# Optimization experiments

Hardware: AMD Instinct MI355X
Metric: run time of the kernel (lower is better)

## Reference

```python
import jax, jax.numpy as jnp
import numpy as np
import math

B, S, E, R = 128, 16, 512, 500  # batch, seq_len, emb_size, relation_num


def setup_inputs() -> dict:
    key = jax.random.key(0)
    ks = jax.random.split(key, 12)
    s = 1.0 / math.sqrt(E)
    emb = jax.random.normal(ks[0], (R + 1, E), jnp.float32) * s
    emb = emb.at[R].set(0.0)  # padding_idx row is zero in torch
    w_ih = jax.random.normal(ks[1], (4 * E, E), jnp.float32) * s
    w_hh = jax.random.normal(ks[2], (4 * E, E), jnp.float32) * s
    b_ih = jax.random.normal(ks[3], (4 * E,), jnp.float32) * s
    b_hh = jax.random.normal(ks[4], (4 * E,), jnp.float32) * s
    fc_w = jax.random.normal(ks[5], (1, E), jnp.float32) * s
    fc_b = jax.random.normal(ks[6], (1,), jnp.float32) * s
    fcq_w = jax.random.normal(ks[7], (E, E), jnp.float32) * s
    fcq_b = jax.random.normal(ks[8], (E,), jnp.float32) * s
    fck_w = jax.random.normal(ks[9], (E, E), jnp.float32) * s
    fck_b = jax.random.normal(ks[10], (E,), jnp.float32) * s
    tokens = jax.random.randint(ks[11], (B, S), 0, R)  # avoid padding idx R
    return dict(tokens=tokens, emb=emb, w_ih=w_ih, w_hh=w_hh, b_ih=b_ih,
                b_hh=b_hh, fc_w=fc_w, fc_b=fc_b, fcq_w=fcq_w, fcq_b=fcq_b,
                fck_w=fck_w, fck_b=fck_b)


def _lstm_pair(x, w_ih, w_hh, b):
    # x: [..., 2, E]; 2-step LSTM from zero state, return final hidden [..., E]
    def cell(xt, h, c):
        g = xt @ w_ih.T + h @ w_hh.T + b
        i, f, gg, o = jnp.split(g, 4, axis=-1)  # torch gate order i,f,g,o
        c = jax.nn.sigmoid(f) * c + jax.nn.sigmoid(i) * jnp.tanh(gg)
        return jax.nn.sigmoid(o) * jnp.tanh(c), c
    z = jnp.zeros_like(x[..., 0, :])
    h1, c1 = cell(x[..., 0, :], z, z)
    h2, _ = cell(x[..., 1, :], h1, c1)
    return h2


def _attention(x, rel_emb, fcq_w, fcq_b, fck_w, fck_b):
    # x: [B,q,E]; keys = [relation embeddings ; x] -> scores [B,q,R+q]
    b = x.shape[0]
    rel = jnp.broadcast_to(rel_emb[None], (b,) + rel_emb.shape)
    kin = jnp.concatenate([rel, x], axis=1)
    k = kin @ fck_w.T + fck_b
    q = x @ fcq_w.T + fcq_b
    return jnp.einsum('bqe,bke->bqk', q, k) / math.sqrt(E)


def _entropy(scores):
    lp = jax.nn.log_softmax(scores, axis=-1)
    return -jnp.sum(jnp.exp(lp) * lp, axis=-1)


def reference(tokens, emb, w_ih, w_hh, b_ih, b_hh, fc_w, fc_b,
              fcq_w, fcq_b, fck_w, fck_b):
    b_lstm = b_ih + b_hh
    rel_emb = emb[:R]  # relation embeddings used as attention keys/values
    cur = emb[tokens]  # [B,S,E]
    bidx = jnp.arange(B)
    losses = []
    for L in range(S, 1, -1):  # lengths processed: S, S-1, ..., 2
        if L > 2:
            # all adjacent pairs, batched 2-step LSTM: [B, L-1, E]
            pairs = jnp.stack([cur[:, :-1], cur[:, 1:]], axis=2)
            h = _lstm_pair(pairs, w_ih, w_hh, b_lstm)
            sc = jax.nn.sigmoid(h @ fc_w.T + fc_b)[..., 0]  # [B, L-1]
            sel = jnp.argmax(sc, axis=-1)  # [B]
            selected = jnp.take_along_axis(h, sel[:, None, None], axis=1)  # [B,1,E]
            scores = _attention(selected, rel_emb, fcq_w, fcq_b, fck_w, fck_b)
            losses.append(_entropy(scores))  # [B,1]
            # weightedAverage: mask is all-False for seq_len==1, plain softmax
            prob = jax.nn.softmax(scores, axis=-1)  # [B,1,R+1]
            all_emb = jnp.concatenate(
                [jnp.broadcast_to(rel_emb[None], (B, R, E)), selected], axis=1)
            merged = jnp.einsum('bqk,bke->bqe', prob, all_emb)[:, 0]  # [B,E]
            # output = inputs.detach().clone(); write merged at sel; drop row sel+1
            base = jax.lax.stop_gradient(cur)
            base = base.at[bidx, sel].set(merged)
            j = jnp.arange(L - 1)[None, :]
            src = j + (j > sel[:, None]).astype(j.dtype)
            cur = jnp.take_along_axis(base, src[:, :, None], axis=1)  # [B,L-1,E]
        else:  # L == 2: plain LSTM over the two tokens
            h = _lstm_pair(cur, w_ih, w_hh, b_lstm)  # [B,E]
            cur = h[:, None, :]
            losses.append(jnp.zeros((B, 1), cur.dtype))
    scores_f = _attention(cur, rel_emb, fcq_w, fcq_b, fck_w, fck_b)  # [B,1,R+1]
    losses.append(_entropy(scores_f))
    loss_tensor = jnp.concatenate(losses, axis=-1)  # [B,S]
    return scores_f[:, 0], loss_tensor
```

## Files before the change

### kernel.cpp

```cpp
#include <hip/hip_runtime.h>
#include <hip/hip_bf16.h>

#define BB 128
#define SS 16
#define EE 512
#define RR 500
#define G4 2048
#define OUT0 64128
#define NSC 501
#define NPAIR 2047
#define NSU 1012

__device__ __forceinline__ float sigm(float x) { return 1.f / (1.f + expf(-x)); }

__device__ float g_blstm[G4];
__device__ float g_blstmr[G4];
__device__ float g_wihr[G4 * EE];
__device__ float g_whhr[G4 * EE];
__device__ float g_fcw[EE + 4];
__device__ float g_qbias[1024];
__device__ float g_Krel[RR * EE];
__device__ float g_cur[BB * SS * EE];
__device__ float g_G[BB * SS * G4];
__device__ float g_h1[BB * SS * EE];
__device__ float g_c1[BB * SS * EE];
__device__ float g_h2[BB * SS * EE];
__device__ float g_sc[BB * SS];
__device__ float g_ent[BB * SS];
__device__ int   g_sel[BB];
__device__ int   g_ord[BB * SS];
__device__ float g_fckwT[EE * EE];
__device__ float g_W2[RR * EE];
__device__ float g_Mx[EE * EE];
__device__ float g_c2[RR + 4];
__device__ float g_v1[EE];
__device__ float g_c0[1];
__device__ float g_su[BB * NSU];

__global__ void k_prep(const float* __restrict__ bih, const float* __restrict__ bhh,
                       const float* __restrict__ fcwv, const float* __restrict__ fcbv,
                       const float* __restrict__ fcqb, const float* __restrict__ fckb) {
    int i = blockIdx.x * blockDim.x + threadIdx.x;
    if (i < G4) g_blstm[i] = bih[i] + bhh[i];
    if (i < EE) {
        g_fcw[i] = fcwv[i];
        g_qbias[i] = fcqb[i];
        g_qbias[EE + i] = fckb[i];
    }
    if (i == 0) g_fcw[EE] = fcbv[0];
    if (i < BB * SS) g_ord[i] = i;
}

__global__ void k_reord(const float* __restrict__ wih, const float* __restrict__ whh) {
    int i = blockIdx.x * blockDim.x + threadIdx.x;
    if (i >= G4 * EE) return;
    int n = i >> 9;
    int k = i & (EE - 1);
    int e = n & (EE - 1);
    int gate = n >> 9;
    int np = 4 * e + gate;
    g_wihr[(size_t)np * EE + k] = wih[i];
    g_whhr[(size_t)np * EE + k] = whh[i];
    if (k == 0) g_blstmr[np] = g_blstm[n];
}

__global__ void k_gather(const int* __restrict__ tok, const float* __restrict__ emb) {
    int i = blockIdx.x * blockDim.x + threadIdx.x;
    if (i >= BB * SS * EE) return;
    int e = i & (EE - 1);
    int r = i >> 9;
    int t = tok[r];
    g_cur[i] = emb[(size_t)t * EE + e];
}

__global__ void k_tr(const float* __restrict__ fckw) {
    int i = blockIdx.x * blockDim.x + threadIdx.x;
    if (i >= EE * EE) return;
    int ep = i >> 9;
    int f = i & (EE - 1);
    g_fckwT[(size_t)f * EE + ep] = fckw[(size_t)ep * EE + f];
}

__global__ __launch_bounds__(512) void k_vprep(const float* __restrict__ fcqw, const float* __restrict__ fckw) {
    __shared__ float sh[512];
    int t = threadIdx.x;
    int blk = blockIdx.x;
    if (blk == 0) {
        float acc = 0.f;
        for (int ep = 0; ep < EE; ep++)
            acc += g_qbias[ep] * fckw[(size_t)ep * EE + t] + g_qbias[EE + ep] * fcqw[(size_t)ep * EE + t];
        g_v1[t] = acc;
    } else if (blk == 1) {
        sh[t] = g_qbias[t] * g_qbias[EE + t];
        __syncthreads();
        for (int s = 256; s > 0; s >>= 1) { if (t < s) sh[t] += sh[t + s]; __syncthreads(); }
        if (t == 0) g_c0[0] = sh[0];
    } else {
        int k = blk - 2;
        sh[t] = g_Krel[(size_t)k * EE + t] * g_qbias[t];
        __syncthreads();
        for (int s = 256; s > 0; s >>= 1) { if (t < s) sh[t] += sh[t + s]; __syncthreads(); }
        if (t == 0) g_c2[k] = sh[0];
    }
}

#define TM 32
#define TN 64
#define TK 32
__device__ __forceinline__ void gemm_dev(
    const float* __restrict__ A, int lda,
    const float* __restrict__ W, int ldw, int wtrans,
    const float* __restrict__ bias, const float* __restrict__ Dadd, int ldd,
    float* __restrict__ C, int ldc, int M, int N, int K)
{
    __shared__ __align__(16) float As[TK][TM + 2];
    __shared__ __align__(16) float Ws[TK][TN + 4];
    int tid = threadIdx.x;
    int mt = blockIdx.y * TM;
    int nt = blockIdx.x * TN;
    int tr = tid >> 4;
    int tc = tid & 15;
    float acc[2][4] = {{0.f,0.f,0.f,0.f},{0.f,0.f,0.f,0.f}};

    int ea = tid * 4;
    int ra = ea >> 5;
    int ka = ea & 31;
    int gmA = mt + ra;
    bool rokA = gmA < M;
    int ew = tid * 8;
    int rw = ew >> 5;
    int kw = ew & 31;
    int gnW = nt + rw;
    bool rokW = gnW < N;

    for (int kt = 0; kt < K; kt += TK) {
        #pragma unroll
        for (int i = 0; i < 4; i++) {
            int gk = kt + ka + i;
            float v = 0.f;
            if (rokA && gk < K) v = A[(size_t)gmA * lda + gk];
            As[ka + i][ra] = v;
        }
        #pragma unroll
        for (int i = 0; i < 8; i++) {
            int gk = kt + kw + i;
            float v = 0.f;
            if (rokW && gk < K)
                v = wtrans ? W[(size_t)gk * ldw + gnW] : W[(size_t)gnW * ldw + gk];
            Ws[kw + i][rw] = v;
        }
        __syncthreads();
        #pragma unroll
        for (int kk = 0; kk < TK; kk++) {
            const float2 a = *(const float2*)&As[kk][2 * tr];
            const float4 w = *(const float4*)&Ws[kk][4 * tc];
            acc[0][0] += a.x * w.x; acc[0][1] += a.x * w.y; acc[0][2] += a.x * w.z; acc[0][3] += a.x * w.w;
            acc[1][0] += a.y * w.x; acc[1][1] += a.y * w.y; acc[1][2] += a.y * w.z; acc[1][3] += a.y * w.w;
        }
        __syncthreads();
    }
    #pragma unroll
    for (int i = 0; i < 2; i++) {
        int gm = mt + 2 * tr + i;
        if (gm >= M) continue;
        #pragma unroll
        for (int j = 0; j < 4; j++) {
            int gn = nt + 4 * tc + j;
            if (gn >= N) continue;
            float v = (i == 0) ? ((j == 0) ? acc[0][0] : (j == 1) ? acc[0][1] : (j == 2) ? acc[0][2] : acc[0][3])
                               : ((j == 0) ? acc[1][0] : (j == 1) ? acc[1][1] : (j == 2) ? acc[1][2] : acc[1][3]);
            if (bias) v += bias[gn];
            if (Dadd) v += Dadd[(size_t)gm * ldd + gn];
            C[(size_t)gm * ldc + gn] = v;
        }
    }
}

#define UM 128
#define UN 128
#define UK 32
template<int MODE>
__global__ __launch_bounds__(256) void kg_bigF() {
    __shared__ __align__(16) float As[UK][UM + 4];
    __shared__ __align__(16) float Ws[UK][UN + 4];
    const float* __restrict__ A = (MODE == 0) ? g_cur : g_h1;
    const float* __restrict__ W = (MODE == 0) ? g_wihr : g_whhr;
    const int M = (MODE == 0) ? (BB * SS) : NPAIR;
    int tid = threadIdx.x;
    int mt = blockIdx.y * UM;
    int nt = blockIdx.x * UN;
    int tr = tid >> 4;
    int tc = tid & 15;
    float acc[8][8] = {};

    int ra = tid & 127;
    int ka = (tid >> 7) << 4;
    int gmA = mt + ra;
    bool rokA = gmA < M;
    const float* Arow = A + (size_t)(rokA ? gmA : 0) * EE;
    const float* Wrow = W + (size_t)(nt + ra) * EE;

    float4 pa[4] = {{0,0,0,0},{0,0,0,0},{0,0,0,0},{0,0,0,0}};
    float4 pw[4];
    #pragma unroll
    for (int j = 0; j < 4; j++) {
        if (rokA) pa[j] = *(const float4*)&Arow[ka + 4 * j];
        pw[j] = *(const float4*)&Wrow[ka + 4 * j];
    }

    for (int kt = 0; kt < EE; kt += UK) {
        __syncthreads();
        #pragma unroll
        for (int j = 0; j < 4; j++) {
            As[ka + 4 * j + 0][ra] = pa[j].x;
            As[ka + 4 * j + 1][ra] = pa[j].y;
            As[ka + 4 * j + 2][ra] = pa[j].z;
            As[ka + 4 * j + 3][ra] = pa[j].w;
            Ws[ka + 4 * j + 0][ra] = pw[j].x;
            Ws[ka + 4 * j + 1][ra] = pw[j].y;
            Ws[ka + 4 * j + 2][ra] = pw[j].z;
            Ws[ka + 4 * j + 3][ra] = pw[j].w;
        }
        __syncthreads();
        if (kt + UK < EE) {
            int k2 = kt + UK + ka;
            #pragma unroll
            for (int j = 0; j < 4; j++) {
                if (rokA) pa[j] = *(const float4*)&Arow[k2 + 4 * j];
                pw[j] = *(const float4*)&Wrow[k2 + 4 * j];
            }
        }
        #pragma unroll
        for (int kk = 0; kk < UK; kk++) {
            const float4 aA = *(const float4*)&As[kk][4 * tr];
            const float4 aB = *(const float4*)&As[kk][64 + 4 * tr];
            const float4 wA = *(const float4*)&Ws[kk][4 * tc];
            const float4 wB = *(const float4*)&Ws[kk][64 + 4 * tc];
            const float am[8] = {aA.x, aA.y, aA.z, aA.w, aB.x, aB.y, aB.z, aB.w};
            const float wn[8] = {wA.x, wA.y, wA.z, wA.w, wB.x, wB.y, wB.z, wB.w};
            #pragma unroll
            for (int i = 0; i < 8; i++)
                #pragma unroll
                for (int j = 0; j < 8; j++)
                    acc[i][j] += am[i] * wn[j];
        }
    }

    int c0 = nt + 4 * tc;
    int c1c = c0 + 64;
    int e0 = (nt >> 2) + tc;
    #pragma unroll
    for (int ri = 0; ri < 8; ri++) {
        int row = (ri < 4) ? (4 * tr + ri) : (60 + 4 * tr + ri);
        int gm = mt + row;
        if (gm >= M) continue;
        float q0x = acc[ri][0], q0y = acc[ri][1], q0z = acc[ri][2], q0w = acc[ri][3];
        float q1x = acc[ri][4], q1y = acc[ri][5], q1z = acc[ri][6], q1w = acc[ri][7];
        if (MODE == 0) {
            const float4 b0 = *(const float4*)&g_blstmr[c0];
            const float4 b1 = *(const float4*)&g_blstmr[c1c];
            q0x += b0.x; q0y += b0.y; q0z += b0.z; q0w += b0.w;
            q1x += b1.x; q1y += b1.y; q1z += b1.z; q1w += b1.w;
            float4 o0 = {q0x, q0y, q0z, q0w};
            float4 o1 = {q1x, q1y, q1z, q1w};
            *(float4*)&g_G[(size_t)gm * G4 + c0]  = o0;
            *(float4*)&g_G[(size_t)gm * G4 + c1c] = o1;
            float cA = sigm(q0x) * tanhf(q0z);
            g_c1[(size_t)gm * EE + e0] = cA;
            g_h1[(size_t)gm * EE + e0] = sigm(q0w) * tanhf(cA);
            float cB = sigm(q1x) * tanhf(q1z);
            g_c1[(size_t)gm * EE + e0 + 16] = cB;
            g_h1[(size_t)gm * EE + e0 + 16] = sigm(q1w) * tanhf(cB);
        } else {
            const float4 d0 = *(const float4*)&g_G[(size_t)(gm + 1) * G4 + c0];
            const float4 d1 = *(const float4*)&g_G[(size_t)(gm + 1) * G4 + c1c];
            q0x += d0.x; q0y += d0.y; q0z += d0.z; q0w += d0.w;
            q1x += d1.x; q1y += d1.y; q1z += d1.z; q1w += d1.w;
            float c1a = g_c1[(size_t)gm * EE + e0];
            float c1b = g_c1[(size_t)gm * EE + e0 + 16];
            float cA = sigm(q0y) * c1a + sigm(q0x) * tanhf(q0z);
            g_h2[(size_t)gm * EE + e0] = sigm(q0w) * tanhf(cA);
            float cB = sigm(q1y) * c1b + sigm(q1x) * tanhf(q1z);
            g_h2[(size_t)gm * EE + e0 + 16] = sigm(q1w) * tanhf(cB);
        }
    }
}

__global__ __launch_bounds__(256) void kg_Krel(const float* __restrict__ emb, const float* __restrict__ fckw) {
    gemm_dev(emb, EE, fckw, EE, 0, g_qbias + EE, nullptr, 0, g_Krel, EE, RR, EE, EE);
}
__global__ __launch_bounds__(256) void kg_W2(const float* __restrict__ fcqw) {
    gemm_dev(g_Krel, EE, fcqw, EE, 1, nullptr, nullptr, 0, g_W2, EE, RR, EE, EE);
}
__global__ __launch_bounds__(256) void kg_Mx(const float* __restrict__ fcqw) {
    gemm_dev(g_fckwT, EE, fcqw, EE, 1, nullptr, nullptr, 0, g_Mx, EE, EE, EE, EE);
}

__global__ __launch_bounds__(256) void k_scI() {
    int m = blockIdx.x;
    int t = threadIdx.x;
    __shared__ float red[256];
    const float* h = g_h2 + (size_t)m * EE;
    float part = h[t] * g_fcw[t] + h[t + 256] * g_fcw[t + 256];
    red[t] = part;
    __syncthreads();
    for (int s = 128; s > 0; s >>= 1) { if (t < s) red[t] += red[t + s]; __syncthreads(); }
    if (t == 0) g_sc[m] = red[0];
}

__global__ __launch_bounds__(256) void k_scP(int L) {
    int m = blockIdx.x;
    int b = m >> 1;
    int tcand = m & 1;
    int s = g_sel[b];
    int p = s - 1 + tcand;
    bool valid = tcand == 0 ? (s >= 1) : (s <= L - 3);
    if (!valid) return;
    int physL = g_ord[b * SS + p];
    int t = threadIdx.x;
    __shared__ float red[256];
    const float* h = g_h2 + (size_t)physL * EE;
    float part = h[t] * g_fcw[t] + h[t + 256] * g_fcw[t + 256];
    red[t] = part;
    __syncthreads();
    for (int s2 = 128; s2 > 0; s2 >>= 1) { if (t < s2) red[t] += red[t + s2]; __syncthreads(); }
    if (t == 0) g_sc[b * SS + p] = red[0];
}

__global__ __launch_bounds__(256) void kg_su(int P) {
    __shared__ __align__(16) float As[TK][TM + 2];
    __shared__ __align__(16) float Ws[TK][TN + 4];
    __shared__ int s_phys[TM];
    int tid = threadIdx.x;
    int mt = blockIdx.y * TM;
    int nt = blockIdx.x * TN;
    int tr = tid >> 4;
    int tc = tid & 15;
    float acc[2][4] = {{0.f,0.f,0.f,0.f},{0.f,0.f,0.f,0.f}};

    if (tid < TM) {
        int b = mt + tid;
        float best = -1e30f; int bi = 0;
        for (int p = 0; p < P; p++) {
            float v = g_sc[b * SS + p];
            if (v > best) { best = v; bi = p; }
        }
        s_phys[tid] = g_ord[b * SS + bi];
        if (blockIdx.x == 0) g_sel[b] = bi;
    }
    __syncthreads();

    int ea = tid * 4;
    int ra = ea >> 5;
    int ka = ea & 31;
    int physA = s_phys[ra];
    int ew = tid * 8;
    int rw = ew >> 5;
    int kw = ew & 31;
    int gnW = nt + rw;
    bool rokW = gnW < NSU;
    const float* Wrow = nullptr;
    if (rokW) Wrow = (gnW < RR) ? (g_W2 + (size_t)gnW * EE) : (g_Mx + (size_t)(gnW - RR) * EE);

    for (int kt = 0; kt < EE; kt += TK) {
        #pragma unroll
        for (int i = 0; i < 4; i++)
            As[ka + i][ra] = g_h2[(size_t)physA * EE + kt + ka + i];
        #pragma unroll
        for (int i = 0; i < 8; i++)
            Ws[kw + i][rw] = rokW ? Wrow[kt + kw + i] : 0.f;
        __syncthreads();
        #pragma unroll
        for (int kk = 0; kk < TK; kk++) {
            const float2 a = *(const float2*)&As[kk][2 * tr];
            const float4 w = *(const float4*)&Ws[kk][4 * tc];
            acc[0][0] += a.x * w.x; acc[0][1] += a.x * w.y; acc[0][2] += a.x * w.z; acc[0][3] += a.x * w.w;
            acc[1][0] += a.y * w.x; acc[1][1] += a.y * w.y; acc[1][2] += a.y * w.z; acc[1][3] += a.y * w.w;
        }
        __syncthreads();
    }
    #pragma unroll
    for (int i = 0; i < 2; i++) {
        int gm = mt + 2 * tr + i;
        #pragma unroll
        for (int j = 0; j < 4; j++) {
            int gn = nt + 4 * tc + j;
            if (gn >= NSU) continue;
            float v = (i == 0) ? ((j == 0) ? acc[0][0] : (j == 1) ? acc[0][1] : (j == 2) ? acc[0][2] : acc[0][3])
                               : ((j == 0) ? acc[1][0] : (j == 1) ? acc[1][1] : (j == 2) ? acc[1][2] : acc[1][3]);
            g_su[(size_t)gm * NSU + gn] = v + (gn < RR ? g_c2[gn] : 0.f);
        }
    }
}

__global__ __launch_bounds__(256) void kg_GiF() {
    __shared__ __align__(16) float As[TK][TM + 2];
    __shared__ __align__(16) float Ws[TK][TN + 4];
    __shared__ int s_phys[TM];
    int tid = threadIdx.x;
    int mt = blockIdx.y * TM;
    int nt = blockIdx.x * TN;
    int tr = tid >> 4;
    int tc = tid & 15;
    float acc[2][4] = {{0.f,0.f,0.f,0.f},{0.f,0.f,0.f,0.f}};

    if (tid < TM) {
        int b = mt + tid;
        s_phys[tid] = g_ord[b * SS + g_sel[b]];
    }
    __syncthreads();

    int ea = tid * 4;
    int ra = ea >> 5;
    int ka = ea & 31;
    int physA = s_phys[ra];
    int ew = tid * 8;
    int rw = ew >> 5;
    int kw = ew & 31;
    int gnW = nt + rw;

    for (int kt = 0; kt < EE; kt += TK) {
        #pragma unroll
        for (int i = 0; i < 4; i++)
            As[ka + i][ra] = g_cur[(size_t)physA * EE + kt + ka + i];
        #pragma unroll
        for (int i = 0; i < 8; i++)
            Ws[kw + i][rw] = g_wihr[(size_t)gnW * EE + kt + kw + i];
        __syncthreads();
        #pragma unroll
        for (int kk = 0; kk < TK; kk++) {
            const float2 a = *(const float2*)&As[kk][2 * tr];
            const float4 w = *(const float4*)&Ws[kk][4 * tc];
            acc[0][0] += a.x * w.x; acc[0][1] += a.x * w.y; acc[0][2] += a.x * w.z; acc[0][3] += a.x * w.w;
            acc[1][0] += a.y * w.x; acc[1][1] += a.y * w.y; acc[1][2] += a.y * w.z; acc[1][3] += a.y * w.w;
        }
        __syncthreads();
    }
    int c0 = nt + 4 * tc;
    int e0 = (nt >> 2) + tc;
    const float4 b4 = *(const float4*)&g_blstmr[c0];
    #pragma unroll
    for (int i = 0; i < 2; i++) {
        int phys = s_phys[2 * tr + i];
        float qx = acc[i][0] + b4.x;
        float qy = acc[i][1] + b4.y;
        float qz = acc[i][2] + b4.z;
        float qw = acc[i][3] + b4.w;
        float4 o = {qx, qy, qz, qw};
        *(float4*)&g_G[(size_t)phys * G4 + c0] = o;
        float cA = sigm(qx) * tanhf(qz);
        g_c1[(size_t)phys * EE + e0] = cA;
        g_h1[(size_t)phys * EE + e0] = sigm(qw) * tanhf(cA);
    }
}

__global__ __launch_bounds__(256) void kg_g2iF(int L) {
    __shared__ __align__(16) float As[TK][TM + 2];
    __shared__ __align__(16) float Ws[TK][TN + 4];
    __shared__ int s_physA[TM];
    __shared__ int s_physD[TM];
    __shared__ int s_val[TM];
    int tid = threadIdx.x;
    int mt = blockIdx.y * TM;
    int nt = blockIdx.x * TN;
    int tr = tid >> 4;
    int tc = tid & 15;
    float acc[2][4] = {{0.f,0.f,0.f,0.f},{0.f,0.f,0.f,0.f}};

    if (tid < TM) {
        int gm = mt + tid;
        int b = gm >> 1;
        int tcand = gm & 1;
        int s = g_sel[b];
        int p = min(max(s - 1 + tcand, 0), 14);
        s_physA[tid] = g_ord[b * SS + p];
        s_physD[tid] = g_ord[b * SS + p + 1];
        s_val[tid] = tcand == 0 ? (s >= 1) : (s <= L - 3);
    }
    __syncthreads();

    int ea = tid * 4;
    int ra = ea >> 5;
    int ka = ea & 31;
    int physA = s_physA[ra];
    int ew = tid * 8;
    int rw = ew >> 5;
    int kw = ew & 31;
    int gnW = nt + rw;

    for (int kt = 0; kt < EE; kt += TK) {
        #pragma unroll
        for (int i = 0; i < 4; i++)
            As[ka + i][ra] = g_h1[(size_t)physA * EE + kt + ka + i];
        #pragma unroll
        for (int i = 0; i < 8; i++)
            Ws[kw + i][rw] = g_whhr[(size_t)gnW * EE + kt + kw + i];
        __syncthreads();
        #pragma unroll
        for (int kk = 0; kk < TK; kk++) {
            const float2 a = *(const float2*)&As[kk][2 * tr];
            const float4 w = *(const float4*)&Ws[kk][4 * tc];
            acc[0][0] += a.x * w.x; acc[0][1] += a.x * w.y; acc[0][2] += a.x * w.z; acc[0][3] += a.x * w.w;
            acc[1][0] += a.y * w.x; acc[1][1] += a.y * w.y; acc[1][2] += a.y * w.z; acc[1][3] += a.y * w.w;
        }
        __syncthreads();
    }
    int c0 = nt + 4 * tc;
    int e0 = (nt >> 2) + tc;
    #pragma unroll
    for (int i = 0; i < 2; i++) {
        int r = 2 * tr + i;
        if (!s_val[r]) continue;
        int pA = s_physA[r];
        int pD = s_physD[r];
        const float4 d4 = *(const float4*)&g_G[(size_t)pD * G4 + c0];
        float qx = acc[i][0] + d4.x;
        float qy = acc[i][1] + d4.y;
        float qz = acc[i][2] + d4.z;
        float qw = acc[i][3] + d4.w;
        float c1v = g_c1[(size_t)pA * EE + e0];
        float cA = sigm(qy) * c1v + sigm(qx) * tanhf(qz);
        g_h2[(size_t)pA * EE + e0] = sigm(qw) * tanhf(cA);
    }
}

__global__ __launch_bounds__(512) void k_smu(int col, int finalFlag, int L,
                                             const float* __restrict__ emb, float* __restrict__ out) {
    int b = blockIdx.x;
    int t = threadIdx.x;
    __shared__ float sh[512];
    __shared__ float srow[NSC];
    __shared__ float s_p500;
    const float* su = g_su + (size_t)b * NSU;
    int s = g_sel[b];
    int phys = g_ord[b * SS + s];
    const float* h2row = g_h2 + (size_t)phys * EE;
    const float isq = 0.044194173824159216f;

    float hv = h2row[t];
    sh[t] = hv * (su[RR + t] + g_v1[t]);
    __syncthreads();
    for (int ss = 256; ss > 0; ss >>= 1) { if (t < ss) sh[t] += sh[t + ss]; __syncthreads(); }
    if (t == 0) srow[RR] = (sh[0] + g_c0[0]) * isq;
    __syncthreads();
    if (t < RR) srow[t] = su[t] * isq;
    __syncthreads();
    float mx = (t < NSC) ? srow[t] : -1e30f;
    sh[t] = mx; __syncthreads();
    for (int ss = 256; ss > 0; ss >>= 1) { if (t < ss) sh[t] = fmaxf(sh[t], sh[t + ss]); __syncthreads(); }
    mx = sh[0]; __syncthreads();
    float zp = (t < NSC) ? expf(srow[t] - mx) : 0.f;
    sh[t] = zp; __syncthreads();
    for (int ss = 256; ss > 0; ss >>= 1) { if (t < ss) sh[t] += sh[t + ss]; __syncthreads(); }
    float lse = mx + logf(sh[0]);
    __syncthreads();
    float p = (t < NSC) ? expf(srow[t] - lse) : 0.f;
    float ep = (t < NSC) ? p * (lse - srow[t]) : 0.f;
    if (finalFlag && t < NSC) out[(size_t)b * NSC + t] = srow[t];
    sh[t] = ep; __syncthreads();
    for (int ss = 256; ss > 0; ss >>= 1) { if (t < ss) sh[t] += sh[t + ss]; __syncthreads(); }
    if (finalFlag) {
        if (t < 16) {
            float v = (t == 15) ? sh[0] : ((t == 14) ? 0.f : g_ent[b * SS + t]);
            out[OUT0 + b * 16 + t] = v;
        }
        return;
    }
    if (t == 0) g_ent[b * SS + col] = sh[0];

    __syncthreads();
    if (t < NSC) srow[t] = p;
    if (t == RR) s_p500 = p;
    __syncthreads();
    float macc = 0.f;
    #pragma unroll 4
    for (int k = 0; k < RR; k++) macc += srow[k] * emb[(size_t)k * EE + t];
    g_cur[(size_t)phys * EE + t] = macc + s_p500 * hv;
    if (t == 0) {
        for (int j = s + 1; j <= L - 2; j++) g_ord[b * SS + j] = g_ord[b * SS + j + 1];
        for (int pp = s + 1; pp <= L - 3; pp++) g_sc[b * SS + pp] = g_sc[b * SS + pp + 1];
    }
}

extern "C" void kernel_launch(void* const* d_in, const int* in_sizes, int n_in,
                              void* d_out, int out_size, void* d_ws, size_t ws_size,
                              hipStream_t stream) {
    const int*   tokens = (const int*)d_in[0];
    const float* emb    = (const float*)d_in[1];
    const float* wih    = (const float*)d_in[2];
    const float* whh    = (const float*)d_in[3];
    const float* bih    = (const float*)d_in[4];
    const float* bhh    = (const float*)d_in[5];
    const float* fcwv   = (const float*)d_in[6];
    const float* fcbv   = (const float*)d_in[7];
    const float* fcqw   = (const float*)d_in[8];
    const float* fcqb   = (const float*)d_in[9];
    const float* fckw   = (const float*)d_in[10];
    const float* fckb   = (const float*)d_in[11];
    float* out = (float*)d_out;

    auto grid32 = [](int M, int N) { return dim3((unsigned)((N + TN - 1) / TN), (unsigned)((M + TM - 1) / TM)); };

    k_prep<<<dim3(8), dim3(256), 0, stream>>>(bih, bhh, fcwv, fcbv, fcqb, fckb);
    k_reord<<<dim3((G4 * EE) / 256), dim3(256), 0, stream>>>(wih, whh);
    kg_Krel<<<grid32(RR, EE), dim3(256), 0, stream>>>(emb, fckw);
    k_tr<<<dim3((EE * EE + 255) / 256), dim3(256), 0, stream>>>(fckw);
    kg_W2<<<grid32(RR, EE), dim3(256), 0, stream>>>(fcqw);
    kg_Mx<<<grid32(EE, EE), dim3(256), 0, stream>>>(fcqw);
    k_vprep<<<dim3(502), dim3(512), 0, stream>>>(fcqw, fckw);
    k_gather<<<dim3((BB * SS * EE + 255) / 256), dim3(256), 0, stream>>>(tokens, emb);

    kg_bigF<0><<<dim3(16, 16), dim3(256), 0, stream>>>();
    kg_bigF<1><<<dim3(16, 16), dim3(256), 0, stream>>>();
    k_scI<<<dim3(NPAIR), dim3(256), 0, stream>>>();

    for (int L = SS; L >= 3; L--) {
        kg_su<<<grid32(BB, NSU), dim3(256), 0, stream>>>(L - 1);
        k_smu<<<dim3(BB), dim3(512), 0, stream>>>(SS - L, 0, L, emb, out);
        kg_GiF<<<grid32(BB, G4), dim3(256), 0, stream>>>();
        kg_g2iF<<<grid32(2 * BB, G4), dim3(256), 0, stream>>>(L);
        k_scP<<<dim3(2 * BB), dim3(256), 0, stream>>>(L);
    }

    kg_su<<<grid32(BB, NSU), dim3(256), 0, stream>>>(1);
    k_smu<<<dim3(BB), dim3(512), 0, stream>>>(15, 1, 2, emb, out);

    (void)in_sizes; (void)n_in; (void)out_size; (void)d_ws; (void)ws_size;
}
```

Before: 1.953 ms.

## Vectorize and register-prefetch GEMM tile loads, halve bigF N-tile

Replaces the scalar, strided global loads in the shared 32x64 GEMM helper and the per-step gate/score GEMMs with float4 loads. These are prefetched into registers for the next K-tile while the current tile is being computed. The fcq weight is pre-transposed once so every GEMM reads W row-major, which removes the strided transposed-load path. The big LSTM input GEMM moves from a 128x128 to a 128x64 tile, doubling block count to improve occupancy at the cost of more A-tile reloads.

```diff
diff --git a/kernel.cpp b/kernel.cpp
--- a/kernel.cpp
+++ b/kernel.cpp
@@ -30,6 +30,7 @@
 __device__ int   g_sel[BB];
 __device__ int   g_ord[BB * SS];
 __device__ float g_fckwT[EE * EE];
+__device__ float g_fcqwT[EE * EE];
 __device__ float g_W2[RR * EE];
 __device__ float g_Mx[EE * EE];
 __device__ float g_c2[RR + 4];
@@ -73,12 +74,13 @@
     g_cur[i] = emb[(size_t)t * EE + e];
 }
 
-__global__ void k_tr(const float* __restrict__ fckw) {
+__global__ void k_tr(const float* __restrict__ fckw, const float* __restrict__ fcqw) {
     int i = blockIdx.x * blockDim.x + threadIdx.x;
     if (i >= EE * EE) return;
     int ep = i >> 9;
     int f = i & (EE - 1);
     g_fckwT[(size_t)f * EE + ep] = fckw[(size_t)ep * EE + f];
+    g_fcqwT[(size_t)f * EE + ep] = fcqw[(size_t)ep * EE + f];
 }
 
 __global__ __launch_bounds__(512) void k_vprep(const float* __restrict__ fcqw, const float* __restrict__ fckw) {
@@ -109,7 +111,7 @@
 #define TK 32
 __device__ __forceinline__ void gemm_dev(
     const float* __restrict__ A, int lda,
-    const float* __restrict__ W, int ldw, int wtrans,
+    const float* __restrict__ W, int ldw,
     const float* __restrict__ bias, const float* __restrict__ Dadd, int ldd,
     float* __restrict__ C, int ldc, int M, int N, int K)
 {
@@ -127,29 +129,27 @@
     int ka = ea & 31;
     int gmA = mt + ra;
     bool rokA = gmA < M;
+    const float* Arow = A + (size_t)(rokA ? gmA : 0) * lda;
     int ew = tid * 8;
     int rw = ew >> 5;
     int kw = ew & 31;
     int gnW = nt + rw;
     bool rokW = gnW < N;
+    const float* Wrow = W + (size_t)(rokW ? gnW : 0) * ldw;
+
+    float4 pa = {0,0,0,0}, pw0 = {0,0,0,0}, pw1 = {0,0,0,0};
+    if (rokA) pa = *(const float4*)&Arow[ka];
+    if (rokW) { pw0 = *(const float4*)&Wrow[kw]; pw1 = *(const float4*)&Wrow[kw + 4]; }
 
     for (int kt = 0; kt < K; kt += TK) {
-        #pragma unroll
-        for (int i = 0; i < 4; i++) {
-            int gk = kt + ka + i;
-            float v = 0.f;
-            if (rokA && gk < K) v = A[(size_t)gmA * lda + gk];
-            As[ka + i][ra] = v;
-        }
-        #pragma unroll
-        for (int i = 0; i < 8; i++) {
-            int gk = kt + kw + i;
-            float v = 0.f;
-            if (rokW && gk < K)
-                v = wtrans ? W[(size_t)gk * ldw + gnW] : W[(size_t)gnW * ldw + gk];
-            Ws[kw + i][rw] = v;
-        }
-        __syncthreads();
+        As[ka + 0][ra] = pa.x; As[ka + 1][ra] = pa.y; As[ka + 2][ra] = pa.z; As[ka + 3][ra] = pa.w;
+        Ws[kw + 0][rw] = pw0.x; Ws[kw + 1][rw] = pw0.y; Ws[kw + 2][rw] = pw0.z; Ws[kw + 3][rw] = pw0.w;
+        Ws[kw + 4][rw] = pw1.x; Ws[kw + 5][rw] = pw1.y; Ws[kw + 6][rw] = pw1.z; Ws[kw + 7][rw] = pw1.w;
+        __syncthreads();
+        if (kt + TK < K) {
+            if (rokA) pa = *(const float4*)&Arow[kt + TK + ka];
+            if (rokW) { pw0 = *(const float4*)&Wrow[kt + TK + kw]; pw1 = *(const float4*)&Wrow[kt + TK + kw + 4]; }
+        }
         #pragma unroll
         for (int kk = 0; kk < TK; kk++) {
             const float2 a = *(const float2*)&As[kk][2 * tr];
@@ -177,7 +177,7 @@
 }
 
 #define UM 128
-#define UN 128
+#define UN 64
 #define UK 32
 template<int MODE>
 __global__ __launch_bounds__(256) void kg_bigF() {
@@ -191,109 +191,97 @@
     int nt = blockIdx.x * UN;
     int tr = tid >> 4;
     int tc = tid & 15;
-    float acc[8][8] = {};
+    float acc[8][4] = {};
 
     int ra = tid & 127;
     int ka = (tid >> 7) << 4;
     int gmA = mt + ra;
     bool rokA = gmA < M;
     const float* Arow = A + (size_t)(rokA ? gmA : 0) * EE;
-    const float* Wrow = W + (size_t)(nt + ra) * EE;
-
-    float4 pa[4] = {{0,0,0,0},{0,0,0,0},{0,0,0,0},{0,0,0,0}};
-    float4 pw[4];
+    int rw = tid & 63;
+    int kw = (tid >> 6) << 3;
+    const float* Wrow = W + (size_t)(nt + rw) * EE;
+
+    float4 pa[4] = {};
+    float4 pw[2];
     #pragma unroll
-    for (int j = 0; j < 4; j++) {
-        if (rokA) pa[j] = *(const float4*)&Arow[ka + 4 * j];
-        pw[j] = *(const float4*)&Wrow[ka + 4 * j];
-    }
+    for (int j = 0; j < 4; j++) if (rokA) pa[j] = *(const float4*)&Arow[ka + 4 * j];
+    #pragma unroll
+    for (int j = 0; j < 2; j++) pw[j] = *(const float4*)&Wrow[kw + 4 * j];
 
     for (int kt = 0; kt < EE; kt += UK) {
-        __syncthreads();
         #pragma unroll
         for (int j = 0; j < 4; j++) {
             As[ka + 4 * j + 0][ra] = pa[j].x;
             As[ka + 4 * j + 1][ra] = pa[j].y;
             As[ka + 4 * j + 2][ra] = pa[j].z;
             As[ka + 4 * j + 3][ra] = pa[j].w;
-            Ws[ka + 4 * j + 0][ra] = pw[j].x;
-            Ws[ka + 4 * j + 1][ra] = pw[j].y;
-            Ws[ka + 4 * j + 2][ra] = pw[j].z;
-            Ws[ka + 4 * j + 3][ra] = pw[j].w;
+        }
+        #pragma unroll
+        for (int j = 0; j < 2; j++) {
+            Ws[kw + 4 * j + 0][rw] = pw[j].x;
+            Ws[kw + 4 * j + 1][rw] = pw[j].y;
+            Ws[kw + 4 * j + 2][rw] = pw[j].z;
+            Ws[kw + 4 * j + 3][rw] = pw[j].w;
         }
         __syncthreads();
         if (kt + UK < EE) {
-            int k2 = kt + UK + ka;
+            int k2 = kt + UK;
             #pragma unroll
-            for (int j = 0; j < 4; j++) {
-                if (rokA) pa[j] = *(const float4*)&Arow[k2 + 4 * j];
-                pw[j] = *(const float4*)&Wrow[k2 + 4 * j];
-            }
+            for (int j = 0; j < 4; j++) if (rokA) pa[j] = *(const float4*)&Arow[k2 + ka + 4 * j];
+            #pragma unroll
+            for (int j = 0; j < 2; j++) pw[j] = *(const float4*)&Wrow[k2 + kw + 4 * j];
         }
         #pragma unroll
         for (int kk = 0; kk < UK; kk++) {
             const float4 aA = *(const float4*)&As[kk][4 * tr];
             const float4 aB = *(const float4*)&As[kk][64 + 4 * tr];
-            const float4 wA = *(const float4*)&Ws[kk][4 * tc];
-            const float4 wB = *(const float4*)&Ws[kk][64 + 4 * tc];
+            const float4 w4 = *(const float4*)&Ws[kk][4 * tc];
             const float am[8] = {aA.x, aA.y, aA.z, aA.w, aB.x, aB.y, aB.z, aB.w};
-            const float wn[8] = {wA.x, wA.y, wA.z, wA.w, wB.x, wB.y, wB.z, wB.w};
+            const float wn[4] = {w4.x, w4.y, w4.z, w4.w};
             #pragma unroll
             for (int i = 0; i < 8; i++)
                 #pragma unroll
-                for (int j = 0; j < 8; j++)
+                for (int j = 0; j < 4; j++)
                     acc[i][j] += am[i] * wn[j];
         }
+        __syncthreads();
     }
 
     int c0 = nt + 4 * tc;
-    int c1c = c0 + 64;
     int e0 = (nt >> 2) + tc;
     #pragma unroll
     for (int ri = 0; ri < 8; ri++) {
         int row = (ri < 4) ? (4 * tr + ri) : (60 + 4 * tr + ri);
         int gm = mt + row;
         if (gm >= M) continue;
-        float q0x = acc[ri][0], q0y = acc[ri][1], q0z = acc[ri][2], q0w = acc[ri][3];
-        float q1x = acc[ri][4], q1y = acc[ri][5], q1z = acc[ri][6], q1w = acc[ri][7];
+        float qx = acc[ri][0], qy = acc[ri][1], qz = acc[ri][2], qw = acc[ri][3];
         if (MODE == 0) {
-            const float4 b0 = *(const float4*)&g_blstmr[c0];
-            const float4 b1 = *(const float4*)&g_blstmr[c1c];
-            q0x += b0.x; q0y += b0.y; q0z += b0.z; q0w += b0.w;
-            q1x += b1.x; q1y += b1.y; q1z += b1.z; q1w += b1.w;
-            float4 o0 = {q0x, q0y, q0z, q0w};
-            float4 o1 = {q1x, q1y, q1z, q1w};
-            *(float4*)&g_G[(size_t)gm * G4 + c0]  = o0;
-            *(float4*)&g_G[(size_t)gm * G4 + c1c] = o1;
-            float cA = sigm(q0x) * tanhf(q0z);
+            const float4 b4 = *(const float4*)&g_blstmr[c0];
+            qx += b4.x; qy += b4.y; qz += b4.z; qw += b4.w;
+            float4 o = {qx, qy, qz, qw};
+            *(float4*)&g_G[(size_t)gm * G4 + c0] = o;
+            float cA = sigm(qx) * tanhf(qz);
             g_c1[(size_t)gm * EE + e0] = cA;
-            g_h1[(size_t)gm * EE + e0] = sigm(q0w) * tanhf(cA);
-            float cB = sigm(q1x) * tanhf(q1z);
-            g_c1[(size_t)gm * EE + e0 + 16] = cB;
-            g_h1[(size_t)gm * EE + e0 + 16] = sigm(q1w) * tanhf(cB);
+            g_h1[(size_t)gm * EE + e0] = sigm(qw) * tanhf(cA);
         } else {
-            const float4 d0 = *(const float4*)&g_G[(size_t)(gm + 1) * G4 + c0];
-            const float4 d1 = *(const float4*)&g_G[(size_t)(gm + 1) * G4 + c1c];
-            q0x += d0.x; q0y += d0.y; q0z += d0.z; q0w += d0.w;
-            q1x += d1.x; q1y += d1.y; q1z += d1.z; q1w += d1.w;
-            float c1a = g_c1[(size_t)gm * EE + e0];
-            float c1b = g_c1[(size_t)gm * EE + e0 + 16];
-            float cA = sigm(q0y) * c1a + sigm(q0x) * tanhf(q0z);
-            g_h2[(size_t)gm * EE + e0] = sigm(q0w) * tanhf(cA);
-            float cB = sigm(q1y) * c1b + sigm(q1x) * tanhf(q1z);
-            g_h2[(size_t)gm * EE + e0 + 16] = sigm(q1w) * tanhf(cB);
+            const float4 d4 = *(const float4*)&g_G[(size_t)(gm + 1) * G4 + c0];
+            qx += d4.x; qy += d4.y; qz += d4.z; qw += d4.w;
+            float c1v = g_c1[(size_t)gm * EE + e0];
+            float cA = sigm(qy) * c1v + sigm(qx) * tanhf(qz);
+            g_h2[(size_t)gm * EE + e0] = sigm(qw) * tanhf(cA);
         }
     }
 }
 
 __global__ __launch_bounds__(256) void kg_Krel(const float* __restrict__ emb, const float* __restrict__ fckw) {
-    gemm_dev(emb, EE, fckw, EE, 0, g_qbias + EE, nullptr, 0, g_Krel, EE, RR, EE, EE);
-}
-__global__ __launch_bounds__(256) void kg_W2(const float* __restrict__ fcqw) {
-    gemm_dev(g_Krel, EE, fcqw, EE, 1, nullptr, nullptr, 0, g_W2, EE, RR, EE, EE);
-}
-__global__ __launch_bounds__(256) void kg_Mx(const float* __restrict__ fcqw) {
-    gemm_dev(g_fckwT, EE, fcqw, EE, 1, nullptr, nullptr, 0, g_Mx, EE, EE, EE, EE);
+    gemm_dev(emb, EE, fckw, EE, g_qbias + EE, nullptr, 0, g_Krel, EE, RR, EE, EE);
+}
+__global__ __launch_bounds__(256) void kg_W2() {
+    gemm_dev(g_Krel, EE, g_fcqwT, EE, nullptr, nullptr, 0, g_W2, EE, RR, EE, EE);
+}
+__global__ __launch_bounds__(256) void kg_Mx() {
+    gemm_dev(g_fckwT, EE, g_fcqwT, EE, nullptr, nullptr, 0, g_Mx, EE, EE, EE, EE);
 }
 
 __global__ __launch_bounds__(256) void k_scI() {
@@ -353,7 +341,7 @@
     int ea = tid * 4;
     int ra = ea >> 5;
     int ka = ea & 31;
-    int physA = s_phys[ra];
+    const float* Arow = g_h2 + (size_t)s_phys[ra] * EE;
     int ew = tid * 8;
     int rw = ew >> 5;
     int kw = ew & 31;
@@ -362,14 +350,19 @@
     const float* Wrow = nullptr;
     if (rokW) Wrow = (gnW < RR) ? (g_W2 + (size_t)gnW * EE) : (g_Mx + (size_t)(gnW - RR) * EE);
 
+    float4 pa = *(const float4*)&Arow[ka];
+    float4 pw0 = {0,0,0,0}, pw1 = {0,0,0,0};
+    if (rokW) { pw0 = *(const float4*)&Wrow[kw]; pw1 = *(const float4*)&Wrow[kw + 4]; }
+
     for (int kt = 0; kt < EE; kt += TK) {
-        #pragma unroll
-        for (int i = 0; i < 4; i++)
-            As[ka + i][ra] = g_h2[(size_t)physA * EE + kt + ka + i];
-        #pragma unroll
-        for (int i = 0; i < 8; i++)
-            Ws[kw + i][rw] = rokW ? Wrow[kt + kw + i] : 0.f;
-        __syncthreads();
+        As[ka + 0][ra] = pa.x; As[ka + 1][ra] = pa.y; As[ka + 2][ra] = pa.z; As[ka + 3][ra] = pa.w;
+        Ws[kw + 0][rw] = pw0.x; Ws[kw + 1][rw] = pw0.y; Ws[kw + 2][rw] = pw0.z; Ws[kw + 3][rw] = pw0.w;
+        Ws[kw + 4][rw] = pw1.x; Ws[kw + 5][rw] = pw1.y; Ws[kw + 6][rw] = pw1.z; Ws[kw + 7][rw] = pw1.w;
+        __syncthreads();
+        if (kt + TK < EE) {
+            pa = *(const float4*)&Arow[kt + TK + ka];
+            if (rokW) { pw0 = *(const float4*)&Wrow[kt + TK + kw]; pw1 = *(const float4*)&Wrow[kt + TK + kw + 4]; }
+        }
         #pragma unroll
         for (int kk = 0; kk < TK; kk++) {
             const float2 a = *(const float2*)&As[kk][2 * tr];
@@ -413,20 +406,26 @@
     int ea = tid * 4;
     int ra = ea >> 5;
     int ka = ea & 31;
-    int physA = s_phys[ra];
+    const float* Arow = g_cur + (size_t)s_phys[ra] * EE;
     int ew = tid * 8;
     int rw = ew >> 5;
     int kw = ew & 31;
-    int gnW = nt + rw;
+    const float* Wrow = g_wihr + (size_t)(nt + rw) * EE;
+
+    float4 pa = *(const float4*)&Arow[ka];
+    float4 pw0 = *(const float4*)&Wrow[kw];
+    float4 pw1 = *(const float4*)&Wrow[kw + 4];
 
     for (int kt = 0; kt < EE; kt += TK) {
-        #pragma unroll
-        for (int i = 0; i < 4; i++)
-            As[ka + i][ra] = g_cur[(size_t)physA * EE + kt + ka + i];
-        #pragma unroll
-        for (int i = 0; i < 8; i++)
-            Ws[kw + i][rw] = g_wihr[(size_t)gnW * EE + kt + kw + i];
-        __syncthreads();
+        As[ka + 0][ra] = pa.x; As[ka + 1][ra] = pa.y; As[ka + 2][ra] = pa.z; As[ka + 3][ra] = pa.w;
+        Ws[kw + 0][rw] = pw0.x; Ws[kw + 1][rw] = pw0.y; Ws[kw + 2][rw] = pw0.z; Ws[kw + 3][rw] = pw0.w;
+        Ws[kw + 4][rw] = pw1.x; Ws[kw + 5][rw] = pw1.y; Ws[kw + 6][rw] = pw1.z; Ws[kw + 7][rw] = pw1.w;
+        __syncthreads();
+        if (kt + TK < EE) {
+            pa = *(const float4*)&Arow[kt + TK + ka];
+            pw0 = *(const float4*)&Wrow[kt + TK + kw];
+            pw1 = *(const float4*)&Wrow[kt + TK + kw + 4];
+        }
         #pragma unroll
         for (int kk = 0; kk < TK; kk++) {
             const float2 a = *(const float2*)&As[kk][2 * tr];
@@ -482,20 +481,26 @@
     int ea = tid * 4;
     int ra = ea >> 5;
     int ka = ea & 31;
-    int physA = s_physA[ra];
+    const float* Arow = g_h1 + (size_t)s_physA[ra] * EE;
     int ew = tid * 8;
     int rw = ew >> 5;
     int kw = ew & 31;
-    int gnW = nt + rw;
+    const float* Wrow = g_whhr + (size_t)(nt + rw) * EE;
+
+    float4 pa = *(const float4*)&Arow[ka];
+    float4 pw0 = *(const float4*)&Wrow[kw];
+    float4 pw1 = *(const float4*)&Wrow[kw + 4];
 
     for (int kt = 0; kt < EE; kt += TK) {
-        #pragma unroll
-        for (int i = 0; i < 4; i++)
-            As[ka + i][ra] = g_h1[(size_t)physA * EE + kt + ka + i];
-        #pragma unroll
-        for (int i = 0; i < 8; i++)
-            Ws[kw + i][rw] = g_whhr[(size_t)gnW * EE + kt + kw + i];
-        __syncthreads();
+        As[ka + 0][ra] = pa.x; As[ka + 1][ra] = pa.y; As[ka + 2][ra] = pa.z; As[ka + 3][ra] = pa.w;
+        Ws[kw + 0][rw] = pw0.x; Ws[kw + 1][rw] = pw0.y; Ws[kw + 2][rw] = pw0.z; Ws[kw + 3][rw] = pw0.w;
+        Ws[kw + 4][rw] = pw1.x; Ws[kw + 5][rw] = pw1.y; Ws[kw + 6][rw] = pw1.z; Ws[kw + 7][rw] = pw1.w;
+        __syncthreads();
+        if (kt + TK < EE) {
+            pa = *(const float4*)&Arow[kt + TK + ka];
+            pw0 = *(const float4*)&Wrow[kt + TK + kw];
+            pw1 = *(const float4*)&Wrow[kt + TK + kw + 4];
+        }
         #pragma unroll
         for (int kk = 0; kk < TK; kk++) {
             const float2 a = *(const float2*)&As[kk][2 * tr];
@@ -554,8 +559,8 @@
     for (int ss = 256; ss > 0; ss >>= 1) { if (t < ss) sh[t] += sh[t + ss]; __syncthreads(); }
     float lse = mx + logf(sh[0]);
     __syncthreads();
-    float p = (t < NSC) ? expf(srow[t] - lse) : 0.f;
-    float ep = (t < NSC) ? p * (lse - srow[t]) : 0.f;
+    float pb = (t < NSC) ? expf(srow[t] - lse) : 0.f;
+    float ep = (t < NSC) ? pb * (lse - srow[t]) : 0.f;
     if (finalFlag && t < NSC) out[(size_t)b * NSC + t] = srow[t];
     sh[t] = ep; __syncthreads();
     for (int ss = 256; ss > 0; ss >>= 1) { if (t < ss) sh[t] += sh[t + ss]; __syncthreads(); }
@@ -569,8 +574,8 @@
     if (t == 0) g_ent[b * SS + col] = sh[0];
 
     __syncthreads();
-    if (t < NSC) srow[t] = p;
-    if (t == RR) s_p500 = p;
+    if (t < NSC) srow[t] = pb;
+    if (t == RR) s_p500 = pb;
     __syncthreads();
     float macc = 0.f;
     #pragma unroll 4
@@ -604,14 +609,14 @@
     k_prep<<<dim3(8), dim3(256), 0, stream>>>(bih, bhh, fcwv, fcbv, fcqb, fckb);
     k_reord<<<dim3((G4 * EE) / 256), dim3(256), 0, stream>>>(wih, whh);
     kg_Krel<<<grid32(RR, EE), dim3(256), 0, stream>>>(emb, fckw);
-    k_tr<<<dim3((EE * EE + 255) / 256), dim3(256), 0, stream>>>(fckw);
-    kg_W2<<<grid32(RR, EE), dim3(256), 0, stream>>>(fcqw);
-    kg_Mx<<<grid32(EE, EE), dim3(256), 0, stream>>>(fcqw);
+    k_tr<<<dim3((EE * EE + 255) / 256), dim3(256), 0, stream>>>(fckw, fcqw);
+    kg_W2<<<grid32(RR, EE), dim3(256), 0, stream>>>();
+    kg_Mx<<<grid32(EE, EE), dim3(256), 0, stream>>>();
     k_vprep<<<dim3(502), dim3(512), 0, stream>>>(fcqw, fckw);
     k_gather<<<dim3((BB * SS * EE + 255) / 256), dim3(256), 0, stream>>>(tokens, emb);
 
-    kg_bigF<0><<<dim3(16, 16), dim3(256), 0, stream>>>();
-    kg_bigF<1><<<dim3(16, 16), dim3(256), 0, stream>>>();
+    kg_bigF<0><<<dim3(32, 16), dim3(256), 0, stream>>>();
+    kg_bigF<1><<<dim3(32, 16), dim3(256), 0, stream>>>();
     k_scI<<<dim3(NPAIR), dim3(256), 0, stream>>>();
 
     for (int L = SS; L >= 3; L--) {
```

Result: faster. 1.704 ms (-12.8%).
